# Performance work log

Hardware: AMD Instinct MI355X
Metric: run time of the kernel (lower is better)

The kernel has to match this reference:

```python
import jax, jax.numpy as jnp
import numpy as np

E = 1280   # embed_dim
H = 16     # num_heads
D = E // H # head_dim = 80
S = 3072   # total tokens


def _rotate_half(x):
    x1, x2 = x[..., : D // 2], x[..., D // 2:]
    return jnp.concatenate((-x2, x1), axis=-1)


def setup_inputs() -> dict:
    key = jax.random.key(0)
    ks = jax.random.split(key, 7)
    x = jax.random.normal(ks[0], (S, E), dtype=jnp.float32)
    # rotary embeddings: cos/sin of random angles, shape (S, head_dim)
    ang = jax.random.uniform(ks[1], (S, D), dtype=jnp.float32) * (2 * np.pi)
    cos = jnp.cos(ang)
    sin = jnp.sin(ang)
    # 8 variable-length segments covering all S tokens
    cu_seqlens = jnp.array([0, 256, 640, 1024, 1536, 1920, 2304, 2688, 3072], dtype=jnp.int32)
    qkv_w = jax.random.normal(ks[2], (3 * E, E), dtype=jnp.float32) * 0.02
    qkv_b = jax.random.normal(ks[3], (3 * E,), dtype=jnp.float32) * 0.02
    proj_w = jax.random.normal(ks[4], (E, E), dtype=jnp.float32) * 0.02
    proj_b = jax.random.normal(ks[5], (E,), dtype=jnp.float32) * 0.02
    return {"x": x, "cu_seqlens": cu_seqlens, "cos": cos, "sin": sin,
            "qkv_w": qkv_w, "qkv_b": qkv_b, "proj_w": proj_w, "proj_b": proj_b}


def reference(x, cu_seqlens, cos, sin, qkv_w, qkv_b, proj_w, proj_b):
    # QKV projection: (S, 3E)
    qkv = x @ qkv_w.T + qkv_b
    q, k, v = jnp.split(qkv, 3, axis=-1)
    q = q.reshape(S, H, D)
    k = k.reshape(S, H, D)
    v = v.reshape(S, H, D)
    # inline RoPE, broadcast over heads (cos/sin: (S,1,D))
    c = cos[:, None, :]
    s = sin[:, None, :]
    q = q * c + _rotate_half(q) * s
    k = k * c + _rotate_half(k) * s
    # block-diagonal varlen attention: tokens attend only within their segment
    seg_ids = jnp.searchsorted(cu_seqlens, jnp.arange(S), side="right")  # (S,)
    mask = seg_ids[:, None] == seg_ids[None, :]                           # (S,S)
    scale = 1.0 / jnp.sqrt(jnp.asarray(D, dtype=q.dtype))
    scores = jnp.einsum("qhd,khd->hqk", q, k) * scale                    # (H,S,S)
    neg = jnp.finfo(scores.dtype).min
    scores = jnp.where(mask[None, :, :], scores, neg)
    attn = jax.nn.softmax(scores, axis=-1)
    out = jnp.einsum("hqk,khd->qhd", attn, v).reshape(S, E)
    return out @ proj_w.T + proj_b
```

## Files before the change

### kernel.cpp

```cpp
#include <hip/hip_runtime.h>
#include <hip/hip_bf16.h>

#define S_LEN 3072
#define E_DIM 1280
#define NH 16
#define HD 80
#define HDP 96
#define QKV_N 3840

typedef unsigned short u16;
typedef unsigned int u32;
typedef __bf16 bf16x8 __attribute__((ext_vector_type(8)));
typedef float f32x4 __attribute__((ext_vector_type(4)));

__device__ __forceinline__ u16 bf16_bits(float f) {
  __hip_bfloat16 b = __float2bfloat16(f);
  return *reinterpret_cast<u16*>(&b);
}
__device__ __forceinline__ float bf16_to_f(u16 u) {
  unsigned int x = ((unsigned int)u) << 16;
  return __uint_as_float(x);
}
__device__ __forceinline__ void gload_lds16(const u16* g, u16* l) {
  __builtin_amdgcn_global_load_lds(
      (const __attribute__((address_space(1))) void*)g,
      (__attribute__((address_space(3))) void*)l, 16, 0, 0);
}
__device__ __forceinline__ int imin(int a, int b) { return a < b ? a : b; }

#define XB_F4    983040
#define WQKV_F4  1228800
#define WPROJ_F4 409600
__global__ __launch_bounds__(256) void f32_to_bf16_3(const float* __restrict__ sx,
                                                     const float* __restrict__ sq,
                                                     const float* __restrict__ sp,
                                                     u16* __restrict__ dst) {
  int i = blockIdx.x * 256 + threadIdx.x;
  float4 v;
  if (i < XB_F4) v = reinterpret_cast<const float4*>(sx)[i];
  else if (i < XB_F4 + WQKV_F4) v = reinterpret_cast<const float4*>(sq)[i - XB_F4];
  else v = reinterpret_cast<const float4*>(sp)[i - XB_F4 - WQKV_F4];
  ushort4 o;
  o.x = bf16_bits(v.x); o.y = bf16_bits(v.y); o.z = bf16_bits(v.z); o.w = bf16_bits(v.w);
  reinterpret_cast<ushort4*>(dst)[i] = o;
}

template<int OUT_F32>
__global__ __launch_bounds__(256) void gemm_nt(const u16* __restrict__ A,
                                               const u16* __restrict__ B,
                                               const float* __restrict__ bias,
                                               void* __restrict__ Cout,
                                               int M, int N, int K, int nbx) {
  __shared__ u16 As[128 * 64];
  __shared__ u16 Bs[128 * 64];
  const int t = threadIdx.x;
  const int lane = t & 63;
  const int wave = t >> 6;
  const int l15 = lane & 15, l4 = lane >> 4;
  const int wm = (wave >> 1) * 64, wn = (wave & 1) * 64;

  const int nwg = gridDim.x;
  const int lg = (blockIdx.x & 7) * (nwg >> 3) + (blockIdx.x >> 3);
  const int m0 = (lg / nbx) * 128, n0 = (lg % nbx) * 128;

  const u16* gA[4];
  const u16* gB[4];
  u16* lA[4];
  u16* lB[4];
  #pragma unroll
  for (int i = 0; i < 4; ++i) {
    const int c = i * 256 + t;
    const int row = c >> 3;
    const int col = ((c & 7) ^ (row & 7)) * 8;
    gA[i] = A + (size_t)(m0 + row) * K + col;
    gB[i] = B + (size_t)(n0 + row) * K + col;
    lA[i] = &As[c * 8];
    lB[i] = &Bs[c * 8];
  }

  int aoff[4][2], boff[4][2];
  #pragma unroll
  for (int i = 0; i < 4; ++i)
    #pragma unroll
    for (int kk = 0; kk < 2; ++kk) {
      aoff[i][kk] = (wm + i * 16 + l15) * 64 + ((kk * 4 + l4) ^ (l15 & 7)) * 8;
      boff[i][kk] = (wn + i * 16 + l15) * 64 + ((kk * 4 + l4) ^ (l15 & 7)) * 8;
    }

  f32x4 acc[4][4] = {};

  const int nk = K >> 6;
  for (int kt = 0; kt < nk; ++kt) {
    const int k0 = kt << 6;
    #pragma unroll
    for (int i = 0; i < 4; ++i) gload_lds16(gA[i] + k0, lA[i]);
    #pragma unroll
    for (int i = 0; i < 4; ++i) gload_lds16(gB[i] + k0, lB[i]);
    __syncthreads();
    bf16x8 af[4][2], bfr[4][2];
    #pragma unroll
    for (int i = 0; i < 4; ++i)
      #pragma unroll
      for (int kk = 0; kk < 2; ++kk) {
        af[i][kk]  = *reinterpret_cast<const bf16x8*>(&As[aoff[i][kk]]);
        bfr[i][kk] = *reinterpret_cast<const bf16x8*>(&Bs[boff[i][kk]]);
      }
    __builtin_amdgcn_s_setprio(1);
    #pragma unroll
    for (int kk = 0; kk < 2; ++kk)
      #pragma unroll
      for (int i = 0; i < 4; ++i)
        #pragma unroll
        for (int j = 0; j < 4; ++j)
          acc[i][j] = __builtin_amdgcn_mfma_f32_16x16x32_bf16(af[i][kk], bfr[j][kk],
                                                              acc[i][j], 0, 0, 0);
    __builtin_amdgcn_s_setprio(0);
    __syncthreads();
  }

  #pragma unroll
  for (int i = 0; i < 4; ++i) {
    #pragma unroll
    for (int j = 0; j < 4; ++j) {
      const int col = n0 + wn + j * 16 + l15;
      const float bv = bias[col];
      const int rowb = m0 + wm + i * 16 + l4 * 4;
      #pragma unroll
      for (int r = 0; r < 4; ++r) {
        float v = acc[i][j][r] + bv;
        if (OUT_F32)
          reinterpret_cast<float*>(Cout)[(size_t)(rowb + r) * N + col] = v;
        else
          reinterpret_cast<u16*>(Cout)[(size_t)(rowb + r) * N + col] = bf16_bits(v);
      }
    }
  }
}

#define ROPE_NB 12288
#define VT_NB   1920
__global__ __launch_bounds__(256) void rope_vt(const u16* __restrict__ qkv,
                                               const float* __restrict__ cosb,
                                               const float* __restrict__ sinb,
                                               u16* __restrict__ qp,
                                               u16* __restrict__ kp,
                                               u16* __restrict__ vt) {
  const int b = blockIdx.x;
  const int t = threadIdx.x;
  if (b < ROPE_NB) {
    const int h = b / 768;
    const int sl = t >> 6;
    const int p = t & 63;
    const int s = (b % 768) * 4 + sl;
    const size_t ib = (size_t)s * QKV_N + h * HD;
    const size_t ob = ((size_t)h * S_LEN + s) * HDP;
    if (p < 40) {
      const float scale = 0.1118033988749895f;
      float q1 = bf16_to_f(qkv[ib + p]);
      float q2 = bf16_to_f(qkv[ib + 40 + p]);
      float k1 = bf16_to_f(qkv[ib + E_DIM + p]);
      float k2 = bf16_to_f(qkv[ib + E_DIM + 40 + p]);
      float c1 = cosb[(size_t)s * HD + p],      s1 = sinb[(size_t)s * HD + p];
      float c2 = cosb[(size_t)s * HD + 40 + p], s2 = sinb[(size_t)s * HD + 40 + p];
      qp[ob + p]      = bf16_bits((q1 * c1 - q2 * s1) * scale);
      qp[ob + 40 + p] = bf16_bits((q2 * c2 + q1 * s2) * scale);
      kp[ob + p]      = bf16_bits(k1 * c1 - k2 * s1);
      kp[ob + 40 + p] = bf16_bits(k2 * c2 + k1 * s2);
    } else if (p < 48) {
      const int pd = HD + (p - 40) * 2;
      qp[ob + pd] = 0; qp[ob + pd + 1] = 0;
      kp[ob + pd] = 0; kp[ob + pd + 1] = 0;
    }
  } else {
    const int idx = (b - ROPE_NB) * 256 + t;
    const int d = idx % HD;
    const int h = (idx / HD) % NH;
    const int sb = idx / (HD * NH);
    const int s0 = sb * 8;
    if (s0 >= S_LEN) return;
    u16 bb[8];
    #pragma unroll
    for (int j = 0; j < 8; ++j)
      bb[j] = qkv[(size_t)(s0 + j) * QKV_N + 2 * E_DIM + h * HD + d];
    uint4 pk;
    pk.x = bb[0] | ((unsigned)bb[1] << 16);
    pk.y = bb[2] | ((unsigned)bb[3] << 16);
    pk.z = bb[4] | ((unsigned)bb[5] << 16);
    pk.w = bb[6] | ((unsigned)bb[7] << 16);
    *reinterpret_cast<uint4*>(&vt[((size_t)h * HD + d) * S_LEN + s0]) = pk;
  }
}

__global__ __launch_bounds__(256) void attn_fwd(const u16* __restrict__ qp,
                                                const u16* __restrict__ kp,
                                                const u16* __restrict__ vt,
                                                const int* __restrict__ cu, int ncu,
                                                u16* __restrict__ ao) {
  __shared__ u16 Pl[4][16][72];

  const int lg = ((blockIdx.x & 7) * 96) + (blockIdx.x >> 3);
  const int h = lg / 48;
  const int q0 = (lg % 48) * 64;

  const int t = threadIdx.x;
  const int wave = t >> 6;
  const int lane = t & 63;
  const int l15 = lane & 15, l4 = lane >> 4;
  const int qr = q0 + wave * 16;

  int lo = 0, hi = S_LEN;
  for (int i = 0; i + 1 < ncu; ++i) {
    int a = cu[i], b = cu[i + 1];
    if (q0 >= a && q0 < b) { lo = a; hi = b; }
  }
  const int nt = (hi - lo + 63) >> 6;

  const u16* qh = qp + (size_t)h * S_LEN * HDP;
  const u16* kh = kp + (size_t)h * S_LEN * HDP;
  const u16* vh = vt + (size_t)h * HD * S_LEN;

  bf16x8 qf[3];
  #pragma unroll
  for (int c = 0; c < 3; ++c)
    qf[c] = *reinterpret_cast<const bf16x8*>(&qh[(size_t)(qr + l15) * HDP + c * 32 + l4 * 8]);

  f32x4 oacc[5] = {};
  float mrow = -INFINITY, lrow = 0.f;
  const float L2E = 1.4426950408889634f;

  int pwr[4];
  #pragma unroll
  for (int f = 0; f < 4; ++f)
    pwr[f] = ((f * 2 + (l4 >> 1)) ^ (l15 & 7)) * 8 + (l4 & 1) * 4;
  int prd[2];
  #pragma unroll
  for (int kc = 0; kc < 2; ++kc)
    prd[kc] = ((kc * 4 + l4) ^ (l15 & 7)) * 8;

  for (int ti = 0; ti < nt; ++ti) {
    const int kb = lo + ti * 64;

    bf16x8 vreg[2][5];
    #pragma unroll
    for (int kc = 0; kc < 2; ++kc)
      #pragma unroll
      for (int df = 0; df < 5; ++df)
        vreg[kc][df] = *reinterpret_cast<const bf16x8*>(
            &vh[(size_t)(df * 16 + l15) * S_LEN + kb + kc * 32 + l4 * 8]);

    f32x4 sc[4];
    #pragma unroll
    for (int f = 0; f < 4; ++f) { f32x4 z = {0.f, 0.f, 0.f, 0.f}; sc[f] = z; }
    __builtin_amdgcn_s_setprio(1);
    #pragma unroll
    for (int f = 0; f < 4; ++f)
      #pragma unroll
      for (int c = 0; c < 3; ++c) {
        bf16x8 kf = *reinterpret_cast<const bf16x8*>(
            &kh[(size_t)(kb + f * 16 + l15) * HDP + c * 32 + l4 * 8]);
        sc[f] = __builtin_amdgcn_mfma_f32_16x16x32_bf16(kf, qf[c], sc[f], 0, 0, 0);
      }
    __builtin_amdgcn_s_setprio(0);

    if (kb + 64 > hi) {
      #pragma unroll
      for (int f = 0; f < 4; ++f)
        #pragma unroll
        for (int r = 0; r < 4; ++r)
          if (kb + f * 16 + l4 * 4 + r >= hi) sc[f][r] = -INFINITY;
    }

    float tm = -INFINITY;
    #pragma unroll
    for (int f = 0; f < 4; ++f)
      #pragma unroll
      for (int r = 0; r < 4; ++r) tm = fmaxf(tm, sc[f][r]);
    tm = fmaxf(tm, __shfl_xor(tm, 16, 64));
    tm = fmaxf(tm, __shfl_xor(tm, 32, 64));

    if (__any(tm > mrow + 8.f)) {
      float mn = fmaxf(mrow, tm);
      float corr = exp2f((mrow - mn) * L2E);
      mrow = mn;
      lrow *= corr;
      #pragma unroll
      for (int df = 0; df < 5; ++df)
        #pragma unroll
        for (int r = 0; r < 4; ++r) oacc[df][r] *= corr;
    }

    float rs = 0.f;
    #pragma unroll
    for (int f = 0; f < 4; ++f) {
      float p0 = exp2f((sc[f][0] - mrow) * L2E);
      float p1 = exp2f((sc[f][1] - mrow) * L2E);
      float p2 = exp2f((sc[f][2] - mrow) * L2E);
      float p3 = exp2f((sc[f][3] - mrow) * L2E);
      rs += (p0 + p1) + (p2 + p3);
      uint2 w;
      w.x = (u32)bf16_bits(p0) | ((u32)bf16_bits(p1) << 16);
      w.y = (u32)bf16_bits(p2) | ((u32)bf16_bits(p3) << 16);
      *reinterpret_cast<uint2*>(&Pl[wave][l15][pwr[f]]) = w;
    }
    rs += __shfl_xor(rs, 16, 64);
    rs += __shfl_xor(rs, 32, 64);
    lrow += rs;

    asm volatile("s_waitcnt lgkmcnt(0)" ::: "memory");

    __builtin_amdgcn_s_setprio(1);
    #pragma unroll
    for (int kc = 0; kc < 2; ++kc) {
      bf16x8 pf = *reinterpret_cast<const bf16x8*>(&Pl[wave][l15][prd[kc]]);
      #pragma unroll
      for (int df = 0; df < 5; ++df)
        oacc[df] = __builtin_amdgcn_mfma_f32_16x16x32_bf16(vreg[kc][df], pf, oacc[df], 0, 0, 0);
    }
    __builtin_amdgcn_s_setprio(0);
  }

  const float inv = 1.0f / lrow;
  #pragma unroll
  for (int df = 0; df < 5; ++df) {
    ushort4 o;
    o.x = bf16_bits(oacc[df][0] * inv);
    o.y = bf16_bits(oacc[df][1] * inv);
    o.z = bf16_bits(oacc[df][2] * inv);
    o.w = bf16_bits(oacc[df][3] * inv);
    *reinterpret_cast<ushort4*>(
        &ao[(size_t)(qr + l15) * E_DIM + h * HD + df * 16 + l4 * 4]) = o;
  }
}

extern "C" void kernel_launch(void* const* d_in, const int* in_sizes, int n_in,
                              void* d_out, int out_size, void* d_ws, size_t ws_size,
                              hipStream_t stream) {
  const float* x      = (const float*)d_in[0];
  const int*   cu     = (const int*)d_in[1];
  const float* cosb   = (const float*)d_in[2];
  const float* sinb   = (const float*)d_in[3];
  const float* qkv_w  = (const float*)d_in[4];
  const float* qkv_b  = (const float*)d_in[5];
  const float* proj_w = (const float*)d_in[6];
  const float* proj_b = (const float*)d_in[7];
  float* out = (float*)d_out;

  u16* xb     = (u16*)d_ws;
  u16* wqkvb  = xb     + (size_t)S_LEN * E_DIM;
  u16* wprojb = wqkvb  + (size_t)3 * E_DIM * E_DIM;
  u16* qkv    = wprojb + (size_t)E_DIM * E_DIM;
  u16* qp     = qkv    + (size_t)S_LEN * QKV_N;
  u16* kp     = qp     + (size_t)NH * S_LEN * HDP;
  u16* vt     = kp     + (size_t)NH * S_LEN * HDP;
  u16* attn   = vt     + (size_t)NH * HD * S_LEN;

  const int nf4 = XB_F4 + WQKV_F4 + WPROJ_F4;
  f32_to_bf16_3<<<nf4 / 256, 256, 0, stream>>>(x, qkv_w, proj_w, xb);

  gemm_nt<0><<<(QKV_N / 128) * (S_LEN / 128), 256, 0, stream>>>(
      xb, wqkvb, qkv_b, qkv, S_LEN, QKV_N, E_DIM, QKV_N / 128);

  rope_vt<<<ROPE_NB + VT_NB, 256, 0, stream>>>(qkv, cosb, sinb, qp, kp, vt);

  attn_fwd<<<NH * (S_LEN / 64), 256, 0, stream>>>(qp, kp, vt, cu, in_sizes[1], attn);

  gemm_nt<1><<<(E_DIM / 128) * (S_LEN / 128), 256, 0, stream>>>(
      attn, wprojb, proj_b, out, S_LEN, E_DIM, E_DIM, E_DIM / 128);
}
```

Baseline: 128.9 us.

## Stage K/V tiles in shared memory with register prefetch in attention

Each block now cooperatively loads 64-row K and V tiles into swizzled shared memory, so the four waves share one global read instead of each loading K and V separately. The next tile is prefetched into registers while the current one is being computed, then written to LDS between two barriers. Launch bounds now request 3 blocks per CU. The cost is extra LDS use, two block-wide syncs per tile and more register pressure.

```diff
diff --git a/kernel.cpp b/kernel.cpp
--- a/kernel.cpp
+++ b/kernel.cpp
@@ -191,11 +191,13 @@
   }
 }
 
-__global__ __launch_bounds__(256) void attn_fwd(const u16* __restrict__ qp,
-                                                const u16* __restrict__ kp,
-                                                const u16* __restrict__ vt,
-                                                const int* __restrict__ cu, int ncu,
-                                                u16* __restrict__ ao) {
+__global__ __launch_bounds__(256, 3) void attn_fwd(const u16* __restrict__ qp,
+                                                   const u16* __restrict__ kp,
+                                                   const u16* __restrict__ vt,
+                                                   const int* __restrict__ cu, int ncu,
+                                                   u16* __restrict__ ao) {
+  __shared__ u16 Ks[64 * 128];
+  __shared__ u16 Vs[80 * 64];
   __shared__ u16 Pl[4][16][72];
 
   const int lg = ((blockIdx.x & 7) * 96) + (blockIdx.x >> 3);
@@ -224,6 +226,42 @@
   for (int c = 0; c < 3; ++c)
     qf[c] = *reinterpret_cast<const bf16x8*>(&qh[(size_t)(qr + l15) * HDP + c * 32 + l4 * 8]);
 
+  int kr[3], kcc[3], kw[3];
+  #pragma unroll
+  for (int i = 0; i < 3; ++i) {
+    const int c2 = i * 256 + t;
+    kr[i] = c2 / 12; kcc[i] = c2 % 12;
+    kw[i] = kr[i] * 128 + ((kcc[i] ^ (kr[i] & 7)) * 8);
+  }
+  int vd[3], vcc[3], vwo[3];
+  #pragma unroll
+  for (int i = 0; i < 3; ++i) {
+    const int c2 = i * 256 + t;
+    vd[i] = c2 >> 3; vcc[i] = c2 & 7;
+    vwo[i] = vd[i] * 64 + ((vcc[i] ^ (vd[i] & 7)) * 8);
+  }
+  const bool v2 = (t < 128);
+
+  {
+    const int kbv = imin(lo, S_LEN - 64);
+    bf16x8 kstg[3], vstg[3];
+    #pragma unroll
+    for (int i = 0; i < 3; ++i)
+      kstg[i] = *reinterpret_cast<const bf16x8*>(
+          &kh[(size_t)imin(lo + kr[i], S_LEN - 1) * HDP + kcc[i] * 8]);
+    #pragma unroll
+    for (int i = 0; i < 2; ++i)
+      vstg[i] = *reinterpret_cast<const bf16x8*>(&vh[(size_t)vd[i] * S_LEN + kbv + vcc[i] * 8]);
+    if (v2)
+      vstg[2] = *reinterpret_cast<const bf16x8*>(&vh[(size_t)vd[2] * S_LEN + kbv + vcc[2] * 8]);
+    #pragma unroll
+    for (int i = 0; i < 3; ++i) *reinterpret_cast<bf16x8*>(&Ks[kw[i]]) = kstg[i];
+    #pragma unroll
+    for (int i = 0; i < 2; ++i) *reinterpret_cast<bf16x8*>(&Vs[vwo[i]]) = vstg[i];
+    if (v2) *reinterpret_cast<bf16x8*>(&Vs[vwo[2]]) = vstg[2];
+    __syncthreads();
+  }
+
   f32x4 oacc[5] = {};
   float mrow = -INFINITY, lrow = 0.f;
   const float L2E = 1.4426950408889634f;
@@ -239,14 +277,22 @@
 
   for (int ti = 0; ti < nt; ++ti) {
     const int kb = lo + ti * 64;
-
-    bf16x8 vreg[2][5];
-    #pragma unroll
-    for (int kc = 0; kc < 2; ++kc)
-      #pragma unroll
-      for (int df = 0; df < 5; ++df)
-        vreg[kc][df] = *reinterpret_cast<const bf16x8*>(
-            &vh[(size_t)(df * 16 + l15) * S_LEN + kb + kc * 32 + l4 * 8]);
+    const bool more = (ti + 1) < nt;
+
+    bf16x8 kstg[3], vstg[3];
+    if (more) {
+      const int kb2 = kb + 64;
+      const int kbv = imin(kb2, S_LEN - 64);
+      #pragma unroll
+      for (int i = 0; i < 3; ++i)
+        kstg[i] = *reinterpret_cast<const bf16x8*>(
+            &kh[(size_t)imin(kb2 + kr[i], S_LEN - 1) * HDP + kcc[i] * 8]);
+      #pragma unroll
+      for (int i = 0; i < 2; ++i)
+        vstg[i] = *reinterpret_cast<const bf16x8*>(&vh[(size_t)vd[i] * S_LEN + kbv + vcc[i] * 8]);
+      if (v2)
+        vstg[2] = *reinterpret_cast<const bf16x8*>(&vh[(size_t)vd[2] * S_LEN + kbv + vcc[2] * 8]);
+    }
 
     f32x4 sc[4];
     #pragma unroll
@@ -257,7 +303,7 @@
       #pragma unroll
       for (int c = 0; c < 3; ++c) {
         bf16x8 kf = *reinterpret_cast<const bf16x8*>(
-            &kh[(size_t)(kb + f * 16 + l15) * HDP + c * 32 + l4 * 8]);
+            &Ks[(f * 16 + l15) * 128 + (((c * 4 + l4) ^ (l15 & 7)) * 8)]);
         sc[f] = __builtin_amdgcn_mfma_f32_16x16x32_bf16(kf, qf[c], sc[f], 0, 0, 0);
       }
     __builtin_amdgcn_s_setprio(0);
@@ -313,10 +359,23 @@
     for (int kc = 0; kc < 2; ++kc) {
       bf16x8 pf = *reinterpret_cast<const bf16x8*>(&Pl[wave][l15][prd[kc]]);
       #pragma unroll
-      for (int df = 0; df < 5; ++df)
-        oacc[df] = __builtin_amdgcn_mfma_f32_16x16x32_bf16(vreg[kc][df], pf, oacc[df], 0, 0, 0);
+      for (int df = 0; df < 5; ++df) {
+        bf16x8 vf = *reinterpret_cast<const bf16x8*>(
+            &Vs[(df * 16 + l15) * 64 + (((kc * 4 + l4) ^ (l15 & 7)) * 8)]);
+        oacc[df] = __builtin_amdgcn_mfma_f32_16x16x32_bf16(vf, pf, oacc[df], 0, 0, 0);
+      }
     }
     __builtin_amdgcn_s_setprio(0);
+
+    if (more) {
+      __syncthreads();
+      #pragma unroll
+      for (int i = 0; i < 3; ++i) *reinterpret_cast<bf16x8*>(&Ks[kw[i]]) = kstg[i];
+      #pragma unroll
+      for (int i = 0; i < 2; ++i) *reinterpret_cast<bf16x8*>(&Vs[vwo[i]]) = vstg[i];
+      if (v2) *reinterpret_cast<bf16x8*>(&Vs[vwo[2]]) = vstg[2];
+      __syncthreads();
+    }
   }
 
   const float inv = 1.0f / lrow;
```

Result: faster. 109.8 us, median of 2 (-14.9%).

## Stage K/V tiles in LDS shared across eight waves with register prefetch

Applied to the files above, without the earlier changes.

The attention kernel now uses 512-thread blocks covering 128 query rows instead of 64. Each 64-key K tile and V tile is loaded cooperatively into XOR-swizzled shared memory, so all eight waves reuse it instead of each wave fetching K and V from global memory. The next tile is prefetched into registers while the current tile is computed, then written to LDS between two barriers. This cuts redundant global/L2 traffic, at the cost of two block-wide syncs per tile, more LDS per block and fewer, larger blocks.

```diff
diff --git a/kernel.cpp b/kernel.cpp
--- a/kernel.cpp
+++ b/kernel.cpp
@@ -191,16 +191,18 @@
   }
 }
 
-__global__ __launch_bounds__(256) void attn_fwd(const u16* __restrict__ qp,
-                                                const u16* __restrict__ kp,
-                                                const u16* __restrict__ vt,
-                                                const int* __restrict__ cu, int ncu,
-                                                u16* __restrict__ ao) {
-  __shared__ u16 Pl[4][16][72];
-
-  const int lg = ((blockIdx.x & 7) * 96) + (blockIdx.x >> 3);
-  const int h = lg / 48;
-  const int q0 = (lg % 48) * 64;
+__global__ __launch_bounds__(512, 4) void attn_fwd(const u16* __restrict__ qp,
+                                                   const u16* __restrict__ kp,
+                                                   const u16* __restrict__ vt,
+                                                   const int* __restrict__ cu, int ncu,
+                                                   u16* __restrict__ ao) {
+  __shared__ u16 Ks[64 * 128];
+  __shared__ u16 Vs[80 * 64];
+  __shared__ u16 Pl[8][16][72];
+
+  const int lg = ((blockIdx.x & 7) * 48) + (blockIdx.x >> 3);
+  const int h = lg / 24;
+  const int q0 = (lg % 24) * 128;
 
   const int t = threadIdx.x;
   const int wave = t >> 6;
@@ -224,6 +226,36 @@
   for (int c = 0; c < 3; ++c)
     qf[c] = *reinterpret_cast<const bf16x8*>(&qh[(size_t)(qr + l15) * HDP + c * 32 + l4 * 8]);
 
+  const int kr0 = t / 12, kc0 = t % 12;
+  const int kw0 = kr0 * 128 + ((kc0 ^ (kr0 & 7)) * 8);
+  const int c1k = 512 + t;
+  const int kr1 = c1k / 12, kc1 = c1k % 12;
+  const int kw1 = kr1 * 128 + ((kc1 ^ (kr1 & 7)) * 8);
+  const bool kdo1 = (t < 256);
+  const int vd0 = t >> 3, vc0 = t & 7;
+  const int vw0 = vd0 * 64 + ((vc0 ^ (vd0 & 7)) * 8);
+  const int vd1 = 64 + (t >> 3), vc1 = t & 7;
+  const int vw1 = vd1 * 64 + ((vc1 ^ (vd1 & 7)) * 8);
+  const bool vdo1 = (t < 128);
+
+  {
+    const int kbv = imin(lo, S_LEN - 64);
+    bf16x8 k0s, k1s, v0s, v1s;
+    k0s = *reinterpret_cast<const bf16x8*>(
+        &kh[(size_t)imin(lo + kr0, S_LEN - 1) * HDP + kc0 * 8]);
+    if (kdo1)
+      k1s = *reinterpret_cast<const bf16x8*>(
+          &kh[(size_t)imin(lo + kr1, S_LEN - 1) * HDP + kc1 * 8]);
+    v0s = *reinterpret_cast<const bf16x8*>(&vh[(size_t)vd0 * S_LEN + kbv + vc0 * 8]);
+    if (vdo1)
+      v1s = *reinterpret_cast<const bf16x8*>(&vh[(size_t)vd1 * S_LEN + kbv + vc1 * 8]);
+    *reinterpret_cast<bf16x8*>(&Ks[kw0]) = k0s;
+    if (kdo1) *reinterpret_cast<bf16x8*>(&Ks[kw1]) = k1s;
+    *reinterpret_cast<bf16x8*>(&Vs[vw0]) = v0s;
+    if (vdo1) *reinterpret_cast<bf16x8*>(&Vs[vw1]) = v1s;
+    __syncthreads();
+  }
+
   f32x4 oacc[5] = {};
   float mrow = -INFINITY, lrow = 0.f;
   const float L2E = 1.4426950408889634f;
@@ -239,14 +271,21 @@
 
   for (int ti = 0; ti < nt; ++ti) {
     const int kb = lo + ti * 64;
-
-    bf16x8 vreg[2][5];
-    #pragma unroll
-    for (int kc = 0; kc < 2; ++kc)
-      #pragma unroll
-      for (int df = 0; df < 5; ++df)
-        vreg[kc][df] = *reinterpret_cast<const bf16x8*>(
-            &vh[(size_t)(df * 16 + l15) * S_LEN + kb + kc * 32 + l4 * 8]);
+    const bool more = (ti + 1) < nt;
+
+    bf16x8 k0s, k1s, v0s, v1s;
+    if (more) {
+      const int kb2 = kb + 64;
+      const int kbv = imin(kb2, S_LEN - 64);
+      k0s = *reinterpret_cast<const bf16x8*>(
+          &kh[(size_t)imin(kb2 + kr0, S_LEN - 1) * HDP + kc0 * 8]);
+      if (kdo1)
+        k1s = *reinterpret_cast<const bf16x8*>(
+            &kh[(size_t)imin(kb2 + kr1, S_LEN - 1) * HDP + kc1 * 8]);
+      v0s = *reinterpret_cast<const bf16x8*>(&vh[(size_t)vd0 * S_LEN + kbv + vc0 * 8]);
+      if (vdo1)
+        v1s = *reinterpret_cast<const bf16x8*>(&vh[(size_t)vd1 * S_LEN + kbv + vc1 * 8]);
+    }
 
     f32x4 sc[4];
     #pragma unroll
@@ -257,7 +296,7 @@
       #pragma unroll
       for (int c = 0; c < 3; ++c) {
         bf16x8 kf = *reinterpret_cast<const bf16x8*>(
-            &kh[(size_t)(kb + f * 16 + l15) * HDP + c * 32 + l4 * 8]);
+            &Ks[(f * 16 + l15) * 128 + (((c * 4 + l4) ^ (l15 & 7)) * 8)]);
         sc[f] = __builtin_amdgcn_mfma_f32_16x16x32_bf16(kf, qf[c], sc[f], 0, 0, 0);
       }
     __builtin_amdgcn_s_setprio(0);
@@ -313,10 +352,22 @@
     for (int kc = 0; kc < 2; ++kc) {
       bf16x8 pf = *reinterpret_cast<const bf16x8*>(&Pl[wave][l15][prd[kc]]);
       #pragma unroll
-      for (int df = 0; df < 5; ++df)
-        oacc[df] = __builtin_amdgcn_mfma_f32_16x16x32_bf16(vreg[kc][df], pf, oacc[df], 0, 0, 0);
+      for (int df = 0; df < 5; ++df) {
+        bf16x8 vf = *reinterpret_cast<const bf16x8*>(
+            &Vs[(df * 16 + l15) * 64 + (((kc * 4 + l4) ^ (l15 & 7)) * 8)]);
+        oacc[df] = __builtin_amdgcn_mfma_f32_16x16x32_bf16(vf, pf, oacc[df], 0, 0, 0);
+      }
     }
     __builtin_amdgcn_s_setprio(0);
+
+    if (more) {
+      __syncthreads();
+      *reinterpret_cast<bf16x8*>(&Ks[kw0]) = k0s;
+      if (kdo1) *reinterpret_cast<bf16x8*>(&Ks[kw1]) = k1s;
+      *reinterpret_cast<bf16x8*>(&Vs[vw0]) = v0s;
+      if (vdo1) *reinterpret_cast<bf16x8*>(&Vs[vw1]) = v1s;
+      __syncthreads();
+    }
   }
 
   const float inv = 1.0f / lrow;
@@ -362,7 +413,7 @@
 
   rope_vt<<<ROPE_NB + VT_NB, 256, 0, stream>>>(qkv, cosb, sinb, qp, kp, vt);
 
-  attn_fwd<<<NH * (S_LEN / 64), 256, 0, stream>>>(qp, kp, vt, cu, in_sizes[1], attn);
+  attn_fwd<<<NH * (S_LEN / 128), 512, 0, stream>>>(qp, kp, vt, cu, in_sizes[1], attn);
 
   gemm_nt<1><<<(E_DIM / 128) * (S_LEN / 128), 256, 0, stream>>>(
       attn, wprojb, proj_b, out, S_LEN, E_DIM, E_DIM, E_DIM / 128);
```

After: 114.0 us. 1.13x faster.
